# Performance work log

Hardware: AMD Instinct MI355X
Metric: run time of the kernel (lower is better)

Reference implementation:

```python
import jax, jax.numpy as jnp
import numpy as np

EPS = 1e-8
M_MARGIN = 0.5  # circle-loss margin m


def _l2norm(x):
    # torch.cosine_similarity clamps the norm product at eps; clamping each norm is equivalent in effect for randn data
    return x / jnp.maximum(jnp.linalg.norm(x, axis=-1, keepdims=True), EPS)


def setup_inputs() -> dict:
    key = jax.random.key(0)
    k1, k2, k3, k4 = jax.random.split(key, 4)
    N, D = 8192, 1024
    return {
        "text_embeddings": jax.random.normal(k1, (N, D), dtype=jnp.float32),
        "text_pos_embeddings": jax.random.normal(k2, (N, D), dtype=jnp.float32),
        "text_neg_embeddings": jax.random.normal(k3, (N, D), dtype=jnp.float32),
        "text_neg_index": jax.random.randint(k4, (N,), 0, N, dtype=jnp.int64 if jax.config.jax_enable_x64 else jnp.int32),
    }


def reference(text_embeddings, text_pos_embeddings, text_neg_embeddings, text_neg_index):
    # use_all_pair=False, mixcse=-1 branch of RetriContrastLoss.forward
    q = _l2norm(text_embeddings)        # [N, D]
    p = _l2norm(text_pos_embeddings)    # [N, D]
    n = _l2norm(text_neg_embeddings)    # [M, D]

    # normalize-then-GEMM == cosine_similarity(unsqueeze(1), unsqueeze(0))
    sim_neg = jnp.einsum("nd,md->nm", q, n)       # [N, M] query-vs-neg cosines
    sim_pos = jnp.sum(q * p, axis=-1)             # [N]    query-vs-pos diagonal cosines
    # NOTE: temperature is never applied in this branch (faithful to source)

    m = M_MARGIN
    # negatives: an = clamp_min(detach(s) + (1+m), 0); s' = an * (s - delta_n), delta_n = -(1-m)
    an = jnp.maximum(jax.lax.stop_gradient(sim_neg) + (1.0 + m), 0.0)
    s_neg = an * (sim_neg + (1.0 - m))
    # positives: ap = clamp_min(-detach(s) + (1+m), 0); s' = -ap * (s - delta_p), delta_p = 1-m
    ap = jnp.maximum(-jax.lax.stop_gradient(sim_pos) + (1.0 + m), 0.0)
    s_pos = -ap * (sim_pos - (1.0 - m))

    # source flattens via boolean mask then logsumexp over dim=0 -> global logsumexp
    lse_neg = jax.scipy.special.logsumexp(s_neg.reshape(-1))
    lse_pos = jax.scipy.special.logsumexp(s_pos)
    return jax.nn.softplus(lse_neg + lse_pos)
```

## Files before the change

kernel.cpp:

```cpp
#include <hip/hip_runtime.h>
#include <hip/hip_bf16.h>
#include <hip/hip_fp8.h>

#define D_K 1024
#define BM 256
#define BN 256
#define ROWB 512
#define KB_ITER 128
#define NT 4

typedef int intx8 __attribute__((ext_vector_type(8)));
typedef float floatx4 __attribute__((ext_vector_type(4)));

__device__ __forceinline__ unsigned int f2fp4(float v) {
    const float a = fabsf(v);
    unsigned int c = (unsigned int)(a >= 0.25f) + (a >= 0.75f) + (a >= 1.25f)
                   + (a >= 1.75f) + (a >= 2.5f) + (a >= 3.5f) + (a >= 5.0f);
    return c | (v < 0.0f ? 8u : 0u);
}

__device__ __forceinline__ void gl_lds16(const void* g, void* l) {
    __builtin_amdgcn_global_load_lds(
        (const __attribute__((address_space(1))) unsigned int*)g,
        (__attribute__((address_space(3))) unsigned int*)l,
        16, 0, 0);
}

__device__ __forceinline__ intx8 ld_frag4(const unsigned char* rowbase, int c, int e) {
    const int4 d = *(const int4*)(rowbase + ((c ^ e) * 16));
    intx8 v;
    v[0] = d.x; v[1] = d.y; v[2] = d.z; v[3] = d.w;
    v[4] = 0; v[5] = 0; v[6] = 0; v[7] = 0;
    return v;
}

__global__ __launch_bounds__(256)
void prep_kernel(const float* __restrict__ q, const float* __restrict__ p,
                 const float* __restrict__ ng,
                 unsigned short* __restrict__ qn, unsigned short* __restrict__ nn,
                 float* __restrict__ posp) {
    const int wid = threadIdx.x >> 6, lane = threadIdx.x & 63;
    const int row = blockIdx.x * 4 + wid;
    const size_t base = (size_t)row * D_K;
    const float4* q4 = (const float4*)(q + base);
    const float4* p4 = (const float4*)(p + base);
    const float4* n4 = (const float4*)(ng + base);

    float4 qa[4], na[4];
    float qq = 0.f, pp = 0.f, qp = 0.f, nn2 = 0.f;
#pragma unroll
    for (int j = 0; j < 4; j++) {
        qa[j] = q4[j * 64 + lane];
        float4 pa = p4[j * 64 + lane];
        na[j] = n4[j * 64 + lane];
        qq += qa[j].x*qa[j].x + qa[j].y*qa[j].y + qa[j].z*qa[j].z + qa[j].w*qa[j].w;
        pp += pa.x*pa.x + pa.y*pa.y + pa.z*pa.z + pa.w*pa.w;
        qp += qa[j].x*pa.x + qa[j].y*pa.y + qa[j].z*pa.z + qa[j].w*pa.w;
        nn2 += na[j].x*na[j].x + na[j].y*na[j].y + na[j].z*na[j].z + na[j].w*na[j].w;
    }
#pragma unroll
    for (int off = 1; off < 64; off <<= 1) {
        qq += __shfl_xor(qq, off);
        pp += __shfl_xor(pp, off);
        qp += __shfl_xor(qp, off);
        nn2 += __shfl_xor(nn2, off);
    }
    const float rq = 32.0f / fmaxf(sqrtf(qq), 1e-8f);
    const float rn = 32.0f / fmaxf(sqrtf(nn2), 1e-8f);

    unsigned short* qr = qn + (size_t)row * 256;
    unsigned short* nr = nn + (size_t)row * 256;
#pragma unroll
    for (int j = 0; j < 4; j++) {
        unsigned int w = f2fp4(qa[j].x * rq) | (f2fp4(qa[j].y * rq) << 4)
                       | (f2fp4(qa[j].z * rq) << 8) | (f2fp4(qa[j].w * rq) << 12);
        qr[j * 64 + lane] = (unsigned short)w;
        w = f2fp4(na[j].x * rn) | (f2fp4(na[j].y * rn) << 4)
          | (f2fp4(na[j].z * rn) << 8) | (f2fp4(na[j].w * rn) << 12);
        nr[j * 64 + lane] = (unsigned short)w;
    }

    if (lane == 0) {
        const float rp = 1.0f / fmaxf(sqrtf(pp), 1e-8f);
        const float sim = qp * (rq / 32.0f) * rp;
        const float ap = fmaxf(1.5f - sim, 0.0f);
        const float sp = -ap * (sim - 0.5f);
        posp[row] = __expf(sp - 4.0f);
    }
}

__global__ __launch_bounds__(512, 2)
void gemm_lse_fp4(const unsigned char* __restrict__ A,
                  const unsigned char* __restrict__ B,
                  float* __restrict__ negp) {
    __shared__ unsigned char smem[2][2][BM * KB_ITER];

    const int tid = threadIdx.x;
    const int wid = tid >> 6;
    const int lane = tid & 63;
    const int tile_m = blockIdx.y * BM;
    const int tile_n = blockIdx.x * BN;

    const int wave_m = (wid & 1) * 128;
    const int wave_n = (wid >> 1) * 64;
    const int quad = lane >> 4;
    const int r = lane & 15;
    const int e = r & 7;

    floatx4 acc[8][4] = {};

    int lds_off[4];
    int src_off[4];
#pragma unroll
    for (int s = 0; s < 4; s++) {
        const int cc = s * 512 + tid;
        const int row = cc >> 3, slot = cc & 7;
        lds_off[s] = cc * 16;
        src_off[s] = row * ROWB + ((slot ^ (row & 7)) * 16);
    }
    const unsigned char* Ab = A + (size_t)tile_m * ROWB;
    const unsigned char* Bb = B + (size_t)tile_n * ROWB;

#pragma unroll
    for (int s = 0; s < 4; s++) {
        gl_lds16(Ab + src_off[s], &smem[0][0][lds_off[s]]);
        gl_lds16(Bb + src_off[s], &smem[0][1][lds_off[s]]);
    }

#pragma unroll
    for (int it = 0; it < NT; ++it) {
        const int buf = it & 1;
        if (it < NT - 1) {
            const int k0b = (it + 1) * KB_ITER;
#pragma unroll
            for (int s = 0; s < 4; s++) {
                gl_lds16(Ab + src_off[s] + k0b, &smem[buf ^ 1][0][lds_off[s]]);
                gl_lds16(Bb + src_off[s] + k0b, &smem[buf ^ 1][1][lds_off[s]]);
            }
            asm volatile("s_waitcnt vmcnt(8)" ::: "memory");
        } else {
            asm volatile("s_waitcnt vmcnt(0)" ::: "memory");
        }
        __builtin_amdgcn_s_barrier();

        const unsigned char* As = &smem[buf][0][0];
        const unsigned char* Bs = &smem[buf][1][0];
#pragma unroll
        for (int t = 0; t < 2; t++) {
            intx8 b[4];
#pragma unroll
            for (int j = 0; j < 4; j++)
                b[j] = ld_frag4(Bs + (size_t)(wave_n + j * 16 + r) * KB_ITER,
                                t * 4 + quad, e);
#pragma unroll
            for (int h = 0; h < 2; h++) {
                intx8 a[4];
#pragma unroll
                for (int i = 0; i < 4; i++)
                    a[i] = ld_frag4(As + (size_t)(wave_m + h * 64 + i * 16 + r) * KB_ITER,
                                    t * 4 + quad, e);
                __builtin_amdgcn_s_setprio(1);
#pragma unroll
                for (int i = 0; i < 4; i++)
#pragma unroll
                    for (int j = 0; j < 4; j++)
                        acc[h * 4 + i][j] = __builtin_amdgcn_mfma_scale_f32_16x16x128_f8f6f4(
                            a[i], b[j], acc[h * 4 + i][j],
                            4, 4,
                            0, 0x7A7A7A7A,
                            0, 0x7A7A7A7A);
                __builtin_amdgcn_s_setprio(0);
            }
        }
        asm volatile("s_waitcnt lgkmcnt(0)" ::: "memory");
        __builtin_amdgcn_sched_barrier(0);
        __builtin_amdgcn_s_barrier();
    }

    float lsum = 0.0f;
#pragma unroll
    for (int i = 0; i < 8; i++)
#pragma unroll
        for (int j = 0; j < 4; j++)
#pragma unroll
            for (int el = 0; el < 4; el++) {
                const float s = acc[i][j][el];
                const float an = fmaxf(s + 1.5f, 0.0f);
                const float sn = an * (s + 0.5f);
                lsum += __expf(sn - 4.0f);
            }
    for (int off = 32; off > 0; off >>= 1) lsum += __shfl_down(lsum, off);
    __shared__ float red[8];
    if (lane == 0) red[wid] = lsum;
    __syncthreads();
    if (tid == 0) {
        float s = 0.0f;
#pragma unroll
        for (int w = 0; w < 8; w++) s += red[w];
        negp[blockIdx.y * gridDim.x + blockIdx.x] = s;
    }
}

__global__ __launch_bounds__(1024)
void finalize_kernel(const float* __restrict__ negp, int n_neg,
                     const float* __restrict__ posp, int n_pos,
                     float* __restrict__ out) {
    double sn = 0.0, sp = 0.0;
    for (int i = threadIdx.x; i < n_neg; i += 1024) sn += (double)negp[i];
    for (int i = threadIdx.x; i < n_pos; i += 1024) sp += (double)posp[i];
    for (int off = 32; off > 0; off >>= 1) {
        sn += __shfl_down(sn, off);
        sp += __shfl_down(sp, off);
    }
    __shared__ double rn[16], rp[16];
    const int wid = threadIdx.x >> 6, lane = threadIdx.x & 63;
    if (lane == 0) { rn[wid] = sn; rp[wid] = sp; }
    __syncthreads();
    if (threadIdx.x == 0) {
        double NS = 0.0, PS = 0.0;
#pragma unroll
        for (int w = 0; w < 16; w++) { NS += rn[w]; PS += rp[w]; }
        const double x = (4.0 + log(NS)) + (4.0 + log(PS));
        const double spl = (x > 30.0) ? x : log1p(exp(x));
        out[0] = (float)spl;
    }
}

extern "C" void kernel_launch(void* const* d_in, const int* in_sizes, int n_in,
                              void* d_out, int out_size, void* d_ws, size_t ws_size,
                              hipStream_t stream) {
    const float* q = (const float*)d_in[0];
    const float* p = (const float*)d_in[1];
    const float* ng = (const float*)d_in[2];

    const int N = in_sizes[3];
    const int D = in_sizes[0] / N;
    const int M = in_sizes[2] / D;

    char* ws = (char*)d_ws;
    unsigned short* qn = (unsigned short*)ws;
    unsigned short* nn = (unsigned short*)(ws + (size_t)N * ROWB);
    float* negp = (float*)(ws + (size_t)(N + M) * ROWB);
    const int n_neg = (M / BN) * (N / BM);
    float* posp = negp + n_neg;

    prep_kernel<<<N / 4, 256, 0, stream>>>(q, p, ng, qn, nn, posp);
    gemm_lse_fp4<<<dim3(M / BN, N / BM), 512, 0, stream>>>(
        (const unsigned char*)qn, (const unsigned char*)nn, negp);
    finalize_kernel<<<1, 1024, 0, stream>>>(negp, n_neg, posp, N, (float*)d_out);
}
```

Baseline: 169.4 us.

## Restructure FP4 GEMM main loop into ping-pong phases with interleaved prefetch

Replaces the per-K-tile loop, which issued all global-to-LDS prefetches up front and then waited, with four phases per tile. Each phase loads its fragments from LDS, then runs 16 scaled MFMAs bracketed by barriers and priority changes. Prefetches of the next A and B tiles are spread across the first two phases, and the wait on global loads is deferred to the end of the tile. The aim is better overlap of LDS reads, global loads and matrix math, at the cost of more barriers per tile.

```diff
diff --git a/kernel.cpp b/kernel.cpp
--- a/kernel.cpp
+++ b/kernel.cpp
@@ -126,54 +126,97 @@
         gl_lds16(Ab + src_off[s], &smem[0][0][lds_off[s]]);
         gl_lds16(Bb + src_off[s], &smem[0][1][lds_off[s]]);
     }
-
-#pragma unroll
-    for (int it = 0; it < NT; ++it) {
-        const int buf = it & 1;
-        if (it < NT - 1) {
-            const int k0b = (it + 1) * KB_ITER;
-#pragma unroll
-            for (int s = 0; s < 4; s++) {
-                gl_lds16(Ab + src_off[s] + k0b, &smem[buf ^ 1][0][lds_off[s]]);
-                gl_lds16(Bb + src_off[s] + k0b, &smem[buf ^ 1][1][lds_off[s]]);
-            }
-            asm volatile("s_waitcnt vmcnt(8)" ::: "memory");
-        } else {
-            asm volatile("s_waitcnt vmcnt(0)" ::: "memory");
-        }
-        __builtin_amdgcn_s_barrier();
-
+    asm volatile("s_waitcnt vmcnt(0)" ::: "memory");
+    __builtin_amdgcn_s_barrier();
+
+#pragma unroll
+    for (int T = 0; T < NT; ++T) {
+        const int buf = T & 1;
         const unsigned char* As = &smem[buf][0][0];
         const unsigned char* Bs = &smem[buf][1][0];
-#pragma unroll
-        for (int t = 0; t < 2; t++) {
-            intx8 b[4];
-#pragma unroll
-            for (int j = 0; j < 4; j++)
-                b[j] = ld_frag4(Bs + (size_t)(wave_n + j * 16 + r) * KB_ITER,
-                                t * 4 + quad, e);
-#pragma unroll
-            for (int h = 0; h < 2; h++) {
-                intx8 a[4];
-#pragma unroll
-                for (int i = 0; i < 4; i++)
-                    a[i] = ld_frag4(As + (size_t)(wave_m + h * 64 + i * 16 + r) * KB_ITER,
-                                    t * 4 + quad, e);
-                __builtin_amdgcn_s_setprio(1);
-#pragma unroll
-                for (int i = 0; i < 4; i++)
-#pragma unroll
-                    for (int j = 0; j < 4; j++)
-                        acc[h * 4 + i][j] = __builtin_amdgcn_mfma_scale_f32_16x16x128_f8f6f4(
-                            a[i], b[j], acc[h * 4 + i][j],
-                            4, 4,
-                            0, 0x7A7A7A7A,
-                            0, 0x7A7A7A7A);
-                __builtin_amdgcn_s_setprio(0);
-            }
+        const int nk = (T + 1) * KB_ITER;
+        intx8 a[4], b[4];
+
+#pragma unroll
+        for (int j = 0; j < 4; j++)
+            b[j] = ld_frag4(Bs + (size_t)(wave_n + j * 16 + r) * KB_ITER, quad, e);
+#pragma unroll
+        for (int i = 0; i < 4; i++)
+            a[i] = ld_frag4(As + (size_t)(wave_m + i * 16 + r) * KB_ITER, quad, e);
+        if (T < NT - 1) {
+#pragma unroll
+            for (int s = 0; s < 4; s++)
+                gl_lds16(Ab + src_off[s] + nk, &smem[buf ^ 1][0][lds_off[s]]);
         }
-        asm volatile("s_waitcnt lgkmcnt(0)" ::: "memory");
-        __builtin_amdgcn_sched_barrier(0);
+        __builtin_amdgcn_s_barrier();
+        asm volatile("s_waitcnt lgkmcnt(0)" ::: "memory");
+        __builtin_amdgcn_s_setprio(1);
+#pragma unroll
+        for (int i = 0; i < 4; i++)
+#pragma unroll
+            for (int j = 0; j < 4; j++)
+                acc[i][j] = __builtin_amdgcn_mfma_scale_f32_16x16x128_f8f6f4(
+                    a[i], b[j], acc[i][j], 4, 4,
+                    0, 0x7A7A7A7A, 0, 0x7A7A7A7A);
+        __builtin_amdgcn_s_setprio(0);
+        __builtin_amdgcn_s_barrier();
+
+#pragma unroll
+        for (int i = 0; i < 4; i++)
+            a[i] = ld_frag4(As + (size_t)(wave_m + 64 + i * 16 + r) * KB_ITER, quad, e);
+        if (T < NT - 1) {
+#pragma unroll
+            for (int s = 0; s < 4; s++)
+                gl_lds16(Bb + src_off[s] + nk, &smem[buf ^ 1][1][lds_off[s]]);
+        }
+        __builtin_amdgcn_s_barrier();
+        asm volatile("s_waitcnt lgkmcnt(0)" ::: "memory");
+        __builtin_amdgcn_s_setprio(1);
+#pragma unroll
+        for (int i = 0; i < 4; i++)
+#pragma unroll
+            for (int j = 0; j < 4; j++)
+                acc[4 + i][j] = __builtin_amdgcn_mfma_scale_f32_16x16x128_f8f6f4(
+                    a[i], b[j], acc[4 + i][j], 4, 4,
+                    0, 0x7A7A7A7A, 0, 0x7A7A7A7A);
+        __builtin_amdgcn_s_setprio(0);
+        __builtin_amdgcn_s_barrier();
+
+#pragma unroll
+        for (int j = 0; j < 4; j++)
+            b[j] = ld_frag4(Bs + (size_t)(wave_n + j * 16 + r) * KB_ITER, 4 + quad, e);
+#pragma unroll
+        for (int i = 0; i < 4; i++)
+            a[i] = ld_frag4(As + (size_t)(wave_m + i * 16 + r) * KB_ITER, 4 + quad, e);
+        __builtin_amdgcn_s_barrier();
+        asm volatile("s_waitcnt lgkmcnt(0)" ::: "memory");
+        __builtin_amdgcn_s_setprio(1);
+#pragma unroll
+        for (int i = 0; i < 4; i++)
+#pragma unroll
+            for (int j = 0; j < 4; j++)
+                acc[i][j] = __builtin_amdgcn_mfma_scale_f32_16x16x128_f8f6f4(
+                    a[i], b[j], acc[i][j], 4, 4,
+                    0, 0x7A7A7A7A, 0, 0x7A7A7A7A);
+        __builtin_amdgcn_s_setprio(0);
+        __builtin_amdgcn_s_barrier();
+
+#pragma unroll
+        for (int i = 0; i < 4; i++)
+            a[i] = ld_frag4(As + (size_t)(wave_m + 64 + i * 16 + r) * KB_ITER, 4 + quad, e);
+        __builtin_amdgcn_s_barrier();
+        asm volatile("s_waitcnt lgkmcnt(0)" ::: "memory");
+        __builtin_amdgcn_s_setprio(1);
+#pragma unroll
+        for (int i = 0; i < 4; i++)
+#pragma unroll
+            for (int j = 0; j < 4; j++)
+                acc[4 + i][j] = __builtin_amdgcn_mfma_scale_f32_16x16x128_f8f6f4(
+                    a[i], b[j], acc[4 + i][j], 4, 4,
+                    0, 0x7A7A7A7A, 0, 0x7A7A7A7A);
+        __builtin_amdgcn_s_setprio(0);
+        if (T < NT - 1)
+            asm volatile("s_waitcnt vmcnt(0)" ::: "memory");
         __builtin_amdgcn_s_barrier();
     }
 
```

Measured after the change: 178.5 us. 1.05x slower.
